# Kernel optimization log

Measured on AMD Instinct MI355X. Metric: run time of the kernel, lower is better.

## Reference

```python
import jax, jax.numpy as jnp
import numpy as np

B = 1024
FEAT = 512
C = 2
H = 256
TAU = 5.0
EPS = 1e-8


def setup_inputs() -> dict:
    key = jax.random.key(0)
    ks = jax.random.split(key, 5)
    X_c = jax.random.normal(ks[0], (B, FEAT), dtype=jnp.float32)
    labels_or_logits = jax.random.normal(ks[1], (B, C), dtype=jnp.float32)
    adj = jax.random.normal(ks[2], (B, B), dtype=jnp.float32)
    # MLP params (torch Linear default-ish init scale)
    W1 = jax.random.normal(ks[3], (FEAT + C, H), dtype=jnp.float32) * (1.0 / np.sqrt(FEAT + C))
    b1 = jnp.zeros((H,), dtype=jnp.float32)
    W2 = jax.random.normal(ks[4], (H, 1), dtype=jnp.float32) * (1.0 / np.sqrt(H))
    b2 = jnp.zeros((1,), dtype=jnp.float32)
    return {"X_c": X_c, "labels_or_logits": labels_or_logits, "adj": adj,
            "W1": W1, "b1": b1, "W2": W2, "b2": b2}


def reference(X_c, labels_or_logits, adj, W1, b1, W2, b2):
    # pairwise absolute feature differences: [B, B, FEAT]
    feat_diff = jnp.abs(X_c[:, None, :] - X_c[None, :, :])
    # logits path (2-D input): softmax over classes
    labels_oh = jax.nn.softmax(labels_or_logits, axis=-1)  # [B, C]
    label_sim = labels_oh[:, None, :] * labels_oh[None, :, :]  # [B, B, C]
    # Split first linear across the concat boundary to avoid concat alloc:
    # cat([feat_diff, label_sim]) @ W1 == feat_diff @ W1[:FEAT] + label_sim @ W1[FEAT:]
    h = (jnp.einsum('ijf,fh->ijh', feat_diff, W1[:FEAT]) +
         jnp.einsum('ijc,ch->ijh', label_sim, W1[FEAT:]) + b1)
    h = jax.nn.gelu(h, approximate=False)
    h_scores = jax.nn.sigmoid(jnp.einsum('ijh,ho->ijo', h, W2)[..., 0] + b2[0])  # [B, B]
    adj_refined = jax.nn.softmax(adj + TAU * jnp.log(h_scores + EPS), axis=-1)
    return adj_refined, h_scores
```

## Files before the change

### kernel.cpp

```cpp
#include <hip/hip_runtime.h>
#include <stdint.h>

#define BN   1024
#define FEATN 512
#define HDIM 256
#define TAUF 5.0f
#define EPSF 1e-8f

typedef __attribute__((ext_vector_type(8))) _Float16 half8;
typedef __attribute__((ext_vector_type(4))) float f32x4;

#if defined(__has_builtin)
#if __has_builtin(__builtin_amdgcn_rcpf)
#define HAVE_RCPF 1
#endif
#if __has_builtin(__builtin_amdgcn_exp2f)
#define HAVE_EXP2F 1
#endif
#endif

#ifdef HAVE_RCPF
__device__ __forceinline__ float fast_rcp(float x) { return __builtin_amdgcn_rcpf(x); }
#else
__device__ __forceinline__ float fast_rcp(float x) { return 1.0f / x; }
#endif

#ifdef HAVE_EXP2F
__device__ __forceinline__ float fast_exp2(float x) { return __builtin_amdgcn_exp2f(x); }
#else
__device__ __forceinline__ float fast_exp2(float x) { return exp2f(x); }
#endif

#define GC1 (-0.102944544f)
#define GC2 (-2.302116228f)
__device__ __forceinline__ float gelu_w2_acc(float x, float w2, float v) {
  float t = x * x;
  float p = fmaf(t, GC1, GC2);
  float q = p * x;
  float e = fast_exp2(q);
  float r = fast_rcp(e + 1.0f);
  return fmaf(x * w2, r, v);
}

#define BAR() asm volatile("s_waitcnt lgkmcnt(0)\n\ts_barrier" ::: "memory")

__global__ __launch_bounds__(256) void prep_kernel(const float* __restrict__ W1,
                                                   const float* __restrict__ b1,
                                                   const float* __restrict__ lg,
                                                   _Float16* __restrict__ w1h,
                                                   float* __restrict__ oh) {
  int b = blockIdx.x, t = threadIdx.x;
  if (b < FEATN) {
    int k = b, n = t;
    w1h[(((k >> 3) * HDIM) + n) * 8 + (k & 7)] = (_Float16)W1[k * HDIM + n];
  } else if (b < FEATN + 4) {
    int i = (b - FEATN) * 256 + t;
    float l0 = lg[2 * i], l1 = lg[2 * i + 1];
    float m = fmaxf(l0, l1);
    float e0 = __expf(l0 - m), e1 = __expf(l1 - m);
    float inv = 1.0f / (e0 + e1);
    oh[2 * i] = e0 * inv;
    oh[2 * i + 1] = e1 * inv;
  } else {
    int koct = b - FEATN - 4;
    half8 hv = (half8){};
    if (koct == 0) {
      hv[0] = (_Float16)W1[512 * HDIM + t];
      hv[1] = (_Float16)W1[513 * HDIM + t];
      hv[2] = (_Float16)b1[t];
    }
    *(half8*)(w1h + 16 * 8192 + (koct * HDIM + t) * 8) = hv;
  }
}

__global__ __launch_bounds__(256, 4) void gemm_kernel(const float* __restrict__ X,
                                                      const _Float16* __restrict__ w1h,
                                                      const float* __restrict__ oh,
                                                      const float* __restrict__ W2,
                                                      const float* __restrict__ b2,
                                                      float* __restrict__ out_hs) {
  __shared__ __align__(16) _Float16 sX[16 * 520];
  __shared__ __align__(16) half8 sA[2][2][4][64];
  __shared__ float sScore[64 * 4];
  __shared__ float sLab0[64], sLab1[64];

  const int tid = threadIdx.x;
  const int L = tid & 63;
  const int w = tid >> 6;

  int bi = blockIdx.y, bj = blockIdx.x;
  if (bj > bi) { bi = 127 - bi; bj = 128 - bj; }
  const int i0 = bi * 8;
  const int j0 = bj * 8;

  #pragma unroll
  for (int it = 0; it < 4; ++it) {
    int idx = tid + it * 256;
    int row = idx >> 6;
    int oc = idx & 63;
    int grow = (row < 8) ? (i0 + row) : (j0 + row - 8);
    const float* gp = X + grow * FEATN + oc * 8;
    float4 a = *(const float4*)gp;
    float4 c = *(const float4*)(gp + 4);
    half8 hv;
    hv[0] = (_Float16)a.x; hv[1] = (_Float16)a.y; hv[2] = (_Float16)a.z; hv[3] = (_Float16)a.w;
    hv[4] = (_Float16)c.x; hv[5] = (_Float16)c.y; hv[6] = (_Float16)c.z; hv[7] = (_Float16)c.w;
    *(half8*)(sX + row * 520 + oc * 8) = hv;
  }
  if (tid < 64) {
    int gi = i0 + (tid >> 3), gj = j0 + (tid & 7);
    sLab0[tid] = oh[2 * gi] * oh[2 * gj];
    sLab1[tid] = oh[2 * gi + 1] * oh[2 * gj + 1];
  }

  const int nl = L & 15;
  const int koct = L >> 4;
  const _Float16* cxi = sX + (2 * w + (nl >> 3)) * 520 + koct * 8;
  const _Float16* cxj = sX + (8 + (L & 7)) * 520 + koct * 8;

  const _Float16* bbase = w1h + ((koct * HDIM) + w * 64 + nl) * 8;

  f32x4 acc[4][4];

  BAR();

  #define CONSTRUCT(kt, buf, st)                                          \
    {                                                                     \
      half8 xi = *(const half8*)(cxi + (kt) * 32);                        \
      half8 xj = *(const half8*)(cxj + (kt) * 32);                        \
      union { half8 h; unsigned u4[4]; } U;                               \
      U.h = xi - xj;                                                      \
      U.u4[0] &= 0x7FFF7FFFu; U.u4[1] &= 0x7FFF7FFFu;                     \
      U.u4[2] &= 0x7FFF7FFFu; U.u4[3] &= 0x7FFF7FFFu;                     \
      sA[buf][st][w][L] = U.h;                                            \
    }

  #define CONSUME_BODY(kt, buf, st, CEXPR)                                \
    {                                                                     \
      half8 afr[4];                                                       \
      _Pragma("unroll")                                                   \
      for (int s = 0; s < 4; ++s) afr[s] = sA[buf][st][s][L];             \
      half8 bfr[4];                                                       \
      _Pragma("unroll")                                                   \
      for (int u = 0; u < 4; ++u)                                         \
        bfr[u] = *(const half8*)(bbase + (kt) * 8192 + u * 128);          \
      _Pragma("unroll")                                                   \
      for (int s = 0; s < 4; ++s)                                         \
        _Pragma("unroll")                                                 \
        for (int u = 0; u < 4; ++u)                                       \
          acc[s][u] = __builtin_amdgcn_mfma_f32_16x16x32_f16(             \
              afr[s], bfr[u], CEXPR, 0, 0, 0);                            \
    }

  #define CONSUME(kt, buf, st)  CONSUME_BODY(kt, buf, st, acc[s][u])
  #define CONSUME0(kt, buf, st) CONSUME_BODY(kt, buf, st, ((f32x4){0.f, 0.f, 0.f, 0.f}))

  CONSTRUCT(0, 0, 0)
  CONSTRUCT(1, 0, 1)
  BAR();

  CONSUME0(0, 0, 0)
  CONSUME(1, 0, 1)
  CONSTRUCT(2, 1, 0)
  CONSTRUCT(3, 1, 1)
  BAR();

  #pragma unroll 2
  for (int t = 1; t < 8; ++t) {
    const int buf = t & 1;
    CONSUME(2 * t, buf, 0)
    CONSUME(2 * t + 1, buf, 1)
    if (t < 7) {
      CONSTRUCT(2 * t + 2, 1 - buf, 0)
      CONSTRUCT(2 * t + 3, 1 - buf, 1)
    }
    BAR();
  }
  #undef CONSTRUCT
  #undef CONSUME
  #undef CONSUME0
  #undef CONSUME_BODY

  {
    half8 bfr[4];
    #pragma unroll
    for (int u = 0; u < 4; ++u)
      bfr[u] = *(const half8*)(bbase + 16 * 8192 + u * 128);
    #pragma unroll
    for (int s = 0; s < 4; ++s) {
      half8 af = (half8){};
      if (koct == 0) {
        int m = s * 16 + nl;
        af[0] = (_Float16)sLab0[m];
        af[1] = (_Float16)sLab1[m];
        af[2] = (_Float16)1.0f;
      }
      #pragma unroll
      for (int u = 0; u < 4; ++u)
        acc[s][u] = __builtin_amdgcn_mfma_f32_16x16x32_f16(af, bfr[u], acc[s][u], 0, 0, 0);
    }
  }

  const int q = L >> 4;
  float ww2[4];
  #pragma unroll
  for (int u = 0; u < 4; ++u) ww2[u] = W2[w * 64 + u * 16 + nl];
  #pragma unroll
  for (int s = 0; s < 4; ++s) {
    #pragma unroll
    for (int r = 0; r < 4; ++r) {
      int m = s * 16 + q * 4 + r;
      float v = 0.f;
      #pragma unroll
      for (int u = 0; u < 4; ++u) v = gelu_w2_acc(acc[s][u][r], ww2[u], v);
      v += __shfl_xor(v, 1, 64);
      v += __shfl_xor(v, 2, 64);
      v += __shfl_xor(v, 4, 64);
      v += __shfl_xor(v, 8, 64);
      if (nl == 0) sScore[m * 4 + w] = v;
    }
  }
  BAR();
  if (tid < 64) {
    float s4 = sScore[tid * 4 + 0] + sScore[tid * 4 + 1] + sScore[tid * 4 + 2] +
               sScore[tid * 4 + 3] + b2[0];
    float e = fast_exp2(s4 * -1.4426950408889634f);
    float hsv = fast_rcp(1.0f + e);
    int r = tid >> 3, c = tid & 7;
    out_hs[(size_t)(i0 + r) * BN + (j0 + c)] = hsv;
    if (i0 != j0) {
      float tv = __shfl(hsv, (c << 3) | r, 64);
      out_hs[(size_t)(j0 + r) * BN + (i0 + c)] = tv;
    }
  }
}

__global__ __launch_bounds__(256) void softmax_kernel(const float* __restrict__ adj,
                                                      const float* __restrict__ hs,
                                                      float* __restrict__ out) {
  int i = blockIdx.x, t = threadIdx.x;
  __shared__ float redm[4];
  __shared__ float reds[4];
  const float TAUL2 = TAUF * 0.69314718056f;
  float l[4];
  float mx = -1e30f;
  #pragma unroll
  for (int k = 0; k < 4; ++k) {
    int j = t + k * 256;
    float lv = adj[(size_t)i * BN + j] + TAUL2 * __log2f(hs[(size_t)i * BN + j] + EPSF);
    l[k] = lv;
    mx = fmaxf(mx, lv);
  }
  #pragma unroll
  for (int o = 1; o <= 32; o <<= 1) mx = fmaxf(mx, __shfl_xor(mx, o, 64));
  if ((t & 63) == 0) redm[t >> 6] = mx;
  __syncthreads();
  mx = fmaxf(fmaxf(redm[0], redm[1]), fmaxf(redm[2], redm[3]));
  float ex[4];
  float se = 0.f;
  #pragma unroll
  for (int k = 0; k < 4; ++k) { ex[k] = __expf(l[k] - mx); se += ex[k]; }
  #pragma unroll
  for (int o = 1; o <= 32; o <<= 1) se += __shfl_xor(se, o, 64);
  if ((t & 63) == 0) reds[t >> 6] = se;
  __syncthreads();
  se = reds[0] + reds[1] + reds[2] + reds[3];
  float inv = fast_rcp(se);
  #pragma unroll
  for (int k = 0; k < 4; ++k) out[(size_t)i * BN + t + k * 256] = ex[k] * inv;
}

extern "C" void kernel_launch(void* const* d_in, const int* in_sizes, int n_in,
                              void* d_out, int out_size, void* d_ws, size_t ws_size,
                              hipStream_t stream) {
  (void)in_sizes; (void)n_in; (void)out_size; (void)ws_size;
  const float* X   = (const float*)d_in[0];
  const float* lg  = (const float*)d_in[1];
  const float* adj = (const float*)d_in[2];
  const float* W1  = (const float*)d_in[3];
  const float* b1  = (const float*)d_in[4];
  const float* W2  = (const float*)d_in[5];
  const float* b2  = (const float*)d_in[6];
  float* out = (float*)d_out;
  _Float16* w1h = (_Float16*)d_ws;
  float* oh = (float*)((char*)d_ws + 17 * 8192 * 2);

  float* out_hs = out + (size_t)BN * BN;

  prep_kernel<<<dim3(FEATN + 8), dim3(256), 0, stream>>>(W1, b1, lg, w1h, oh);
  gemm_kernel<<<dim3(65, 128), dim3(256), 0, stream>>>(X, w1h, oh, W2, b2, out_hs);
  softmax_kernel<<<dim3(BN), dim3(256), 0, stream>>>(adj, out_hs, out);
}
```

Measured before the change: 237.6 us.

## Build |xi-xj| A-fragments in registers per wave instead of shared staging

Each wave now computes all four A fragments for its MFMAs directly from the X tile in shared memory, rather than having each wave construct one fragment, store it to a double-buffered shared array, and sync. This removes the sA staging buffer and all barriers inside the K loop. In exchange every wave redoes the subtract/abs work four times and issues more LDS reads of X rows.

```diff
diff --git a/kernel.cpp b/kernel.cpp
--- a/kernel.cpp
+++ b/kernel.cpp
@@ -80,7 +80,6 @@
                                                       const float* __restrict__ b2,
                                                       float* __restrict__ out_hs) {
   __shared__ __align__(16) _Float16 sX[16 * 520];
-  __shared__ __align__(16) half8 sA[2][2][4][64];
   __shared__ float sScore[64 * 4];
   __shared__ float sLab0[64], sLab1[64];
 
@@ -115,7 +114,7 @@
 
   const int nl = L & 15;
   const int koct = L >> 4;
-  const _Float16* cxi = sX + (2 * w + (nl >> 3)) * 520 + koct * 8;
+  const _Float16* cxi = sX + (nl >> 3) * 520 + koct * 8;
   const _Float16* cxj = sX + (8 + (L & 7)) * 520 + koct * 8;
 
   const _Float16* bbase = w1h + ((koct * HDIM) + w * 64 + nl) * 8;
@@ -124,62 +123,32 @@
 
   BAR();
 
-  #define CONSTRUCT(kt, buf, st)                                          \
+  #define STEP_BODY(kt, CEXPR)                                            \
     {                                                                     \
-      half8 xi = *(const half8*)(cxi + (kt) * 32);                        \
-      half8 xj = *(const half8*)(cxj + (kt) * 32);                        \
-      union { half8 h; unsigned u4[4]; } U;                               \
-      U.h = xi - xj;                                                      \
-      U.u4[0] &= 0x7FFF7FFFu; U.u4[1] &= 0x7FFF7FFFu;                     \
-      U.u4[2] &= 0x7FFF7FFFu; U.u4[3] &= 0x7FFF7FFFu;                     \
-      sA[buf][st][w][L] = U.h;                                            \
-    }
-
-  #define CONSUME_BODY(kt, buf, st, CEXPR)                                \
-    {                                                                     \
-      half8 afr[4];                                                       \
-      _Pragma("unroll")                                                   \
-      for (int s = 0; s < 4; ++s) afr[s] = sA[buf][st][s][L];             \
       half8 bfr[4];                                                       \
       _Pragma("unroll")                                                   \
       for (int u = 0; u < 4; ++u)                                         \
         bfr[u] = *(const half8*)(bbase + (kt) * 8192 + u * 128);          \
+      half8 xj = *(const half8*)(cxj + (kt) * 32);                        \
       _Pragma("unroll")                                                   \
-      for (int s = 0; s < 4; ++s)                                         \
+      for (int s = 0; s < 4; ++s) {                                       \
+        half8 xi = *(const half8*)(cxi + s * 1040 + (kt) * 32);           \
+        union { half8 h; unsigned u4[4]; } U;                             \
+        U.h = xi - xj;                                                    \
+        U.u4[0] &= 0x7FFF7FFFu; U.u4[1] &= 0x7FFF7FFFu;                   \
+        U.u4[2] &= 0x7FFF7FFFu; U.u4[3] &= 0x7FFF7FFFu;                   \
         _Pragma("unroll")                                                 \
         for (int u = 0; u < 4; ++u)                                       \
           acc[s][u] = __builtin_amdgcn_mfma_f32_16x16x32_f16(             \
-              afr[s], bfr[u], CEXPR, 0, 0, 0);                            \
-    }
-
-  #define CONSUME(kt, buf, st)  CONSUME_BODY(kt, buf, st, acc[s][u])
-  #define CONSUME0(kt, buf, st) CONSUME_BODY(kt, buf, st, ((f32x4){0.f, 0.f, 0.f, 0.f}))
-
-  CONSTRUCT(0, 0, 0)
-  CONSTRUCT(1, 0, 1)
-  BAR();
-
-  CONSUME0(0, 0, 0)
-  CONSUME(1, 0, 1)
-  CONSTRUCT(2, 1, 0)
-  CONSTRUCT(3, 1, 1)
-  BAR();
-
+              U.h, bfr[u], CEXPR, 0, 0, 0);                               \
+      }                                                                   \
+    }
+
+  STEP_BODY(0, ((f32x4){0.f, 0.f, 0.f, 0.f}))
   #pragma unroll 2
-  for (int t = 1; t < 8; ++t) {
-    const int buf = t & 1;
-    CONSUME(2 * t, buf, 0)
-    CONSUME(2 * t + 1, buf, 1)
-    if (t < 7) {
-      CONSTRUCT(2 * t + 2, 1 - buf, 0)
-      CONSTRUCT(2 * t + 3, 1 - buf, 1)
-    }
-    BAR();
-  }
-  #undef CONSTRUCT
-  #undef CONSUME
-  #undef CONSUME0
-  #undef CONSUME_BODY
+  for (int kt = 1; kt < 16; ++kt)
+    STEP_BODY(kt, acc[s][u])
+  #undef STEP_BODY
 
   {
     half8 bfr[4];
```

New measurement: 256.8 us. 8.1% more time.

## Enlarge pair tile to 16x8 with 8 waves splitting hidden dim

Applied to the files above, without the earlier changes.

The GEMM kernel now processes 16 i-rows by 8 j-columns per block with 512 threads. Each of 8 waves covers 32 hidden units and all 128 pairs, so every W1 fragment loaded from global memory feeds twice as many MFMAs. The triangular block mapping is rewritten for the rectangular tiles, and the transposed store now writes directly instead of going through a shuffle. The wider block raises register and LDS pressure per block, and the new mapping may redundantly compute some diagonal tiles.

```diff
diff --git a/kernel.cpp b/kernel.cpp
--- a/kernel.cpp
+++ b/kernel.cpp
@@ -73,32 +73,34 @@
   }
 }
 
-__global__ __launch_bounds__(256, 4) void gemm_kernel(const float* __restrict__ X,
+__global__ __launch_bounds__(512, 4) void gemm_kernel(const float* __restrict__ X,
                                                       const _Float16* __restrict__ w1h,
                                                       const float* __restrict__ oh,
                                                       const float* __restrict__ W2,
                                                       const float* __restrict__ b2,
                                                       float* __restrict__ out_hs) {
-  __shared__ __align__(16) _Float16 sX[16 * 520];
-  __shared__ __align__(16) half8 sA[2][2][4][64];
-  __shared__ float sScore[64 * 4];
-  __shared__ float sLab0[64], sLab1[64];
+  __shared__ __align__(16) _Float16 sX[24 * 520];
+  __shared__ __align__(16) half8 sA[2][2][8][64];
+  __shared__ float sScore[128 * 8];
+  __shared__ float sLab0[128], sLab1[128];
 
   const int tid = threadIdx.x;
   const int L = tid & 63;
   const int w = tid >> 6;
 
-  int bi = blockIdx.y, bj = blockIdx.x;
-  if (bj > bi) { bi = 127 - bi; bj = 128 - bj; }
-  const int i0 = bi * 8;
+  int x = blockIdx.x, y = blockIdx.y;
+  int bi, bj;
+  if (x <= 2 * y + 1) { bi = y; bj = x; }
+  else { bi = 63 - y; bj = 129 - x; }
+  const int i0 = bi * 16;
   const int j0 = bj * 8;
 
   #pragma unroll
-  for (int it = 0; it < 4; ++it) {
-    int idx = tid + it * 256;
+  for (int it = 0; it < 3; ++it) {
+    int idx = tid + it * 512;
     int row = idx >> 6;
     int oc = idx & 63;
-    int grow = (row < 8) ? (i0 + row) : (j0 + row - 8);
+    int grow = (row < 16) ? (i0 + row) : (j0 + row - 16);
     const float* gp = X + grow * FEATN + oc * 8;
     float4 a = *(const float4*)gp;
     float4 c = *(const float4*)(gp + 4);
@@ -107,7 +109,7 @@
     hv[4] = (_Float16)c.x; hv[5] = (_Float16)c.y; hv[6] = (_Float16)c.z; hv[7] = (_Float16)c.w;
     *(half8*)(sX + row * 520 + oc * 8) = hv;
   }
-  if (tid < 64) {
+  if (tid < 128) {
     int gi = i0 + (tid >> 3), gj = j0 + (tid & 7);
     sLab0[tid] = oh[2 * gi] * oh[2 * gj];
     sLab1[tid] = oh[2 * gi + 1] * oh[2 * gj + 1];
@@ -116,11 +118,11 @@
   const int nl = L & 15;
   const int koct = L >> 4;
   const _Float16* cxi = sX + (2 * w + (nl >> 3)) * 520 + koct * 8;
-  const _Float16* cxj = sX + (8 + (L & 7)) * 520 + koct * 8;
-
-  const _Float16* bbase = w1h + ((koct * HDIM) + w * 64 + nl) * 8;
-
-  f32x4 acc[4][4];
+  const _Float16* cxj = sX + (16 + (L & 7)) * 520 + koct * 8;
+
+  const _Float16* bbase = w1h + ((koct * HDIM) + 32 * w + nl) * 8;
+
+  f32x4 acc[8][2];
 
   BAR();
 
@@ -135,25 +137,36 @@
       sA[buf][st][w][L] = U.h;                                            \
     }
 
-  #define CONSUME_BODY(kt, buf, st, CEXPR)                                \
+  #define CONSUME_BODY(kt, buf, st, CEXPR0, CEXPR)                        \
     {                                                                     \
-      half8 afr[4];                                                       \
+      half8 bfr[2];                                                       \
+      bfr[0] = *(const half8*)(bbase + (kt) * 8192);                      \
+      bfr[1] = *(const half8*)(bbase + (kt) * 8192 + 128);                \
+      half8 af0[4];                                                       \
       _Pragma("unroll")                                                   \
-      for (int s = 0; s < 4; ++s) afr[s] = sA[buf][st][s][L];             \
-      half8 bfr[4];                                                       \
-      _Pragma("unroll")                                                   \
-      for (int u = 0; u < 4; ++u)                                         \
-        bfr[u] = *(const half8*)(bbase + (kt) * 8192 + u * 128);          \
+      for (int s = 0; s < 4; ++s) af0[s] = sA[buf][st][s][L];             \
       _Pragma("unroll")                                                   \
       for (int s = 0; s < 4; ++s)                                         \
         _Pragma("unroll")                                                 \
-        for (int u = 0; u < 4; ++u)                                       \
+        for (int u = 0; u < 2; ++u)                                       \
           acc[s][u] = __builtin_amdgcn_mfma_f32_16x16x32_f16(             \
-              afr[s], bfr[u], CEXPR, 0, 0, 0);                            \
-    }
-
-  #define CONSUME(kt, buf, st)  CONSUME_BODY(kt, buf, st, acc[s][u])
-  #define CONSUME0(kt, buf, st) CONSUME_BODY(kt, buf, st, ((f32x4){0.f, 0.f, 0.f, 0.f}))
+              af0[s], bfr[u], CEXPR0, 0, 0, 0);                           \
+      half8 af1[4];                                                       \
+      _Pragma("unroll")                                                   \
+      for (int s = 0; s < 4; ++s) af1[s] = sA[buf][st][4 + s][L];         \
+      _Pragma("unroll")                                                   \
+      for (int s = 0; s < 4; ++s)                                         \
+        _Pragma("unroll")                                                 \
+        for (int u = 0; u < 2; ++u)                                       \
+          acc[4 + s][u] = __builtin_amdgcn_mfma_f32_16x16x32_f16(         \
+              af1[s], bfr[u], CEXPR, 0, 0, 0);                            \
+    }
+
+  #define CONSUME(kt, buf, st)                                            \
+    CONSUME_BODY(kt, buf, st, acc[s][u], acc[4 + s][u])
+  #define CONSUME0(kt, buf, st)                                           \
+    CONSUME_BODY(kt, buf, st, ((f32x4){0.f, 0.f, 0.f, 0.f}),              \
+                 ((f32x4){0.f, 0.f, 0.f, 0.f}))
 
   CONSTRUCT(0, 0, 0)
   CONSTRUCT(1, 0, 1)
@@ -182,12 +195,11 @@
   #undef CONSUME_BODY
 
   {
-    half8 bfr[4];
+    half8 bfr[2];
+    bfr[0] = *(const half8*)(bbase + 16 * 8192);
+    bfr[1] = *(const half8*)(bbase + 16 * 8192 + 128);
     #pragma unroll
-    for (int u = 0; u < 4; ++u)
-      bfr[u] = *(const half8*)(bbase + 16 * 8192 + u * 128);
-    #pragma unroll
-    for (int s = 0; s < 4; ++s) {
+    for (int s = 0; s < 8; ++s) {
       half8 af = (half8){};
       if (koct == 0) {
         int m = s * 16 + nl;
@@ -196,42 +208,40 @@
         af[2] = (_Float16)1.0f;
       }
       #pragma unroll
-      for (int u = 0; u < 4; ++u)
+      for (int u = 0; u < 2; ++u)
         acc[s][u] = __builtin_amdgcn_mfma_f32_16x16x32_f16(af, bfr[u], acc[s][u], 0, 0, 0);
     }
   }
 
   const int q = L >> 4;
-  float ww2[4];
-  #pragma unroll
-  for (int u = 0; u < 4; ++u) ww2[u] = W2[w * 64 + u * 16 + nl];
-  #pragma unroll
-  for (int s = 0; s < 4; ++s) {
+  float ww2[2];
+  #pragma unroll
+  for (int u = 0; u < 2; ++u) ww2[u] = W2[32 * w + u * 16 + nl];
+  #pragma unroll
+  for (int s = 0; s < 8; ++s) {
     #pragma unroll
     for (int r = 0; r < 4; ++r) {
       int m = s * 16 + q * 4 + r;
       float v = 0.f;
       #pragma unroll
-      for (int u = 0; u < 4; ++u) v = gelu_w2_acc(acc[s][u][r], ww2[u], v);
+      for (int u = 0; u < 2; ++u) v = gelu_w2_acc(acc[s][u][r], ww2[u], v);
       v += __shfl_xor(v, 1, 64);
       v += __shfl_xor(v, 2, 64);
       v += __shfl_xor(v, 4, 64);
       v += __shfl_xor(v, 8, 64);
-      if (nl == 0) sScore[m * 4 + w] = v;
+      if (nl == 0) sScore[m * 8 + w] = v;
     }
   }
   BAR();
-  if (tid < 64) {
-    float s4 = sScore[tid * 4 + 0] + sScore[tid * 4 + 1] + sScore[tid * 4 + 2] +
-               sScore[tid * 4 + 3] + b2[0];
-    float e = fast_exp2(s4 * -1.4426950408889634f);
+  if (tid < 128) {
+    float s8 = sScore[tid * 8 + 0] + sScore[tid * 8 + 1] + sScore[tid * 8 + 2] +
+               sScore[tid * 8 + 3] + sScore[tid * 8 + 4] + sScore[tid * 8 + 5] +
+               sScore[tid * 8 + 6] + sScore[tid * 8 + 7] + b2[0];
+    float e = fast_exp2(s8 * -1.4426950408889634f);
     float hsv = fast_rcp(1.0f + e);
     int r = tid >> 3, c = tid & 7;
     out_hs[(size_t)(i0 + r) * BN + (j0 + c)] = hsv;
-    if (i0 != j0) {
-      float tv = __shfl(hsv, (c << 3) | r, 64);
-      out_hs[(size_t)(j0 + r) * BN + (i0 + c)] = tv;
-    }
+    out_hs[(size_t)(j0 + c) * BN + (i0 + r)] = hsv;
   }
 }
 
@@ -288,6 +298,6 @@
   float* out_hs = out + (size_t)BN * BN;
 
   prep_kernel<<<dim3(FEATN + 8), dim3(256), 0, stream>>>(W1, b1, lg, w1h, oh);
-  gemm_kernel<<<dim3(65, 128), dim3(256), 0, stream>>>(X, w1h, oh, W2, b2, out_hs);
+  gemm_kernel<<<dim3(65, 64), dim3(512), 0, stream>>>(X, w1h, oh, W2, b2, out_hs);
   softmax_kernel<<<dim3(BN), dim3(256), 0, stream>>>(adj, out_hs, out);
 }
```

Result: slower. 249.0 us (+4.8%).
